# Performance work log

Measured on AMD Instinct MI355X. Metric: run time of the kernel, lower is better.

Reference implementation:

```python
import jax, jax.numpy as jnp
import numpy as np

N = 50000
E = 800000
NFEAT, NHID, NCLASS = 256, 128, 32


def setup_inputs() -> dict:
    key = jax.random.key(0)
    ks = jax.random.split(key, 8)
    x = jax.random.normal(ks[0], (N, NFEAT), dtype=jnp.float32)
    edge_src = jax.random.randint(ks[1], (E,), 0, N, dtype=jnp.int32)
    edge_dst = jax.random.randint(ks[2], (E,), 0, N, dtype=jnp.int32)
    edge_weight = jax.random.uniform(ks[3], (E,), dtype=jnp.float32)
    # Linear layer params (torch Linear: y = x @ W.T + b); store as [in, out]
    s1 = 1.0 / np.sqrt(NFEAT)
    s2 = 1.0 / np.sqrt(NHID)
    W1 = jax.random.uniform(ks[4], (NFEAT, NHID), jnp.float32, -s1, s1)
    b1 = jax.random.uniform(ks[5], (NHID,), jnp.float32, -s1, s1)
    W2 = jax.random.uniform(ks[6], (NHID, NCLASS), jnp.float32, -s2, s2)
    b2 = jax.random.uniform(ks[7], (NCLASS,), jnp.float32, -s2, s2)
    return {"x": x, "edge_src": edge_src, "edge_dst": edge_dst,
            "edge_weight": edge_weight, "W1": W1, "b1": b1, "W2": W2, "b2": b2}


def spmm(edge_src, edge_dst, edge_weight, h):
    # out[dst] += w * h[src]  -- sparse adjacency @ dense features
    msgs = edge_weight[:, None] * h[edge_src]          # [E, F]
    return jax.ops.segment_sum(msgs, edge_dst, num_segments=N)


def reference(x, edge_src, edge_dst, edge_weight, W1, b1, W2, b2):
    # GCN layer 1: Linear -> SpMM -> ReLU (dropout inactive in eval mode)
    h = x @ W1 + b1                                    # [N, NHID]
    h = spmm(edge_src, edge_dst, edge_weight, h)
    h = jax.nn.relu(h)
    # GCN layer 2: Linear -> SpMM
    h = h @ W2 + b2                                    # [N, NCLASS]
    out = spmm(edge_src, edge_dst, edge_weight, h)
    return out
```

## Files before the change

kernel.cpp:

```cpp
#include <hip/hip_runtime.h>

#define NFEAT 256
#define NHID 128
#define NCLASS 32

typedef __attribute__((ext_vector_type(8))) short short8;
typedef __attribute__((ext_vector_type(4))) float f32x4;
typedef __attribute__((ext_vector_type(4))) int int4v;

static __device__ __forceinline__ unsigned short f2bf(float f) {
    unsigned u = __float_as_uint(f);
    unsigned r = (u + 0x7fffu + ((u >> 16) & 1u)) >> 16;
    return (unsigned short)r;
}
static __device__ __forceinline__ float bf_lo(unsigned d) {
    return __uint_as_float(d << 16);
}
static __device__ __forceinline__ float bf_hi(unsigned d) {
    return __uint_as_float(d & 0xffff0000u);
}

__global__ __launch_bounds__(256) void prep_kernel(
    const float* __restrict__ W1, unsigned short* __restrict__ W1t,
    const int* __restrict__ dst, int* __restrict__ bkt_partial, int E, int shift)
{
    const int tid = threadIdx.x;
    if (blockIdx.x < 128) {
        int o = blockIdx.x * 256 + tid;
        int c = o >> 8, k = o & 255;
        W1t[o] = f2bf(W1[(size_t)k * NHID + c]);
    } else {
        __shared__ int h[256];
        const int kb = blockIdx.x - 128;
        h[tid] = 0;
        __syncthreads();
        for (int e = kb * 256 + tid; e < E; e += 256 * 256)
            atomicAdd(&h[dst[e] >> shift], 1);
        __syncthreads();
        bkt_partial[kb * 256 + tid] = h[tid];
    }
}

__global__ __launch_bounds__(256) void gemm1_mfma_kernel(
    const float* __restrict__ x, const unsigned short* __restrict__ W1t,
    const float* __restrict__ b1, unsigned short* __restrict__ h1b, int N)
{
    __shared__ unsigned short wt[128 * 256];
    __shared__ unsigned short xs[64 * 64];

    const int tid = threadIdx.x;
    const int lane = tid & 63;
    const int wv = tid >> 6;
    const int row0 = blockIdx.x * 64;
    const int l15 = lane & 15;
    const int l47 = lane >> 4;
    const int r7 = lane & 7;

    {
        const int4v* src = (const int4v*)W1t;
#pragma unroll
        for (int j = 0; j < 16; ++j) {
            int si = tid + j * 256;
            int c = si >> 5, s = si & 31;
            int sp = (s & 24) | ((s & 7) ^ (c & 7));
            int4v v = src[si];
            *(int4v*)&wt[c * 256 + sp * 8] = v;
        }
    }

    auto stage_x = [&](int t) {
#pragma unroll
        for (int j = 0; j < 2; ++j) {
            int si = tid + j * 256;
            int r = si >> 3, s = si & 7;
            int row = row0 + r;
            float4 v0 = make_float4(0.f, 0.f, 0.f, 0.f), v1 = v0;
            if (row < N) {
                const float4* xp = (const float4*)&x[(size_t)row * NFEAT + t * 64 + s * 8];
                v0 = xp[0]; v1 = xp[1];
            }
            int w0 = f2bf(v0.x) | ((unsigned)f2bf(v0.y) << 16);
            int w1 = f2bf(v0.z) | ((unsigned)f2bf(v0.w) << 16);
            int w2 = f2bf(v1.x) | ((unsigned)f2bf(v1.y) << 16);
            int w3 = f2bf(v1.z) | ((unsigned)f2bf(v1.w) << 16);
            int sp = s ^ (r & 7);
            int4v pv; pv[0] = w0; pv[1] = w1; pv[2] = w2; pv[3] = w3;
            *(int4v*)&xs[r * 64 + sp * 8] = pv;
        }
    };

    f32x4 acc[8];
#pragma unroll
    for (int cf = 0; cf < 8; ++cf)
#pragma unroll
        for (int r = 0; r < 4; ++r) acc[cf][r] = 0.f;

    stage_x(0);
    __syncthreads();

    const int arow = wv * 16 + l15;
#pragma unroll
    for (int t = 0; t < 4; ++t) {
        short8 af[2];
#pragma unroll
        for (int kf = 0; kf < 2; ++kf) {
            int slot = (kf * 4 + l47) ^ r7;
            af[kf] = *(const short8*)&xs[arow * 64 + slot * 8];
        }
#pragma unroll
        for (int cf = 0; cf < 8; ++cf) {
            const int brow = cf * 16 + l15;
#pragma unroll
            for (int kf = 0; kf < 2; ++kf) {
                int slot = t * 8 + ((kf * 4 + l47) ^ r7);
                short8 bfr = *(const short8*)&wt[brow * 256 + slot * 8];
                acc[cf] = __builtin_amdgcn_mfma_f32_16x16x32_bf16(af[kf], bfr, acc[cf], 0, 0, 0);
            }
        }
        __syncthreads();
        if (t < 3) {
            stage_x(t + 1);
            __syncthreads();
        }
    }

#pragma unroll
    for (int cf = 0; cf < 8; ++cf) {
        float bias = b1[cf * 16 + l15];
#pragma unroll
        for (int r = 0; r < 4; ++r) {
            int row = row0 + wv * 16 + l47 * 4 + r;
            if (row < N)
                h1b[(size_t)row * NHID + cf * 16 + l15] = f2bf(acc[cf][r] + bias);
        }
    }
}

__global__ __launch_bounds__(256) void bucket_scan_kernel(
    const int* __restrict__ bkt_partial, int* __restrict__ bkt_base,
    int* __restrict__ bkt_cursor)
{
    __shared__ int s[256];
    const int t = threadIdx.x;
    int v = 0;
    for (int k = 0; k < 256; ++k) v += bkt_partial[k * 256 + t];
    s[t] = v;
    __syncthreads();
    for (int off = 1; off < 256; off <<= 1) {
        int tv = (t >= off) ? s[t - off] : 0;
        __syncthreads();
        s[t] += tv;
        __syncthreads();
    }
    int excl = s[t] - v;
    bkt_base[t] = excl;
    bkt_cursor[t] = excl;
    if (t == 255) bkt_base[256] = s[255];
}

#define SC_EPT 16
__global__ __launch_bounds__(256) void bucket_scatter_kernel(
    const int* __restrict__ src, const int* __restrict__ dst,
    const float* __restrict__ w, int* __restrict__ bkt_cursor,
    uint2* __restrict__ bkt_edges, int E, int shift)
{
    __shared__ int h[256];
    __shared__ int base[256];
    const int tid = threadIdx.x;
    const int e0 = blockIdx.x * (256 * SC_EPT);
    h[tid] = 0;
    __syncthreads();
#pragma unroll
    for (int j = 0; j < SC_EPT; ++j) {
        int e = e0 + tid + j * 256;
        if (e < E) atomicAdd(&h[dst[e] >> shift], 1);
    }
    __syncthreads();
    int c = h[tid];
    base[tid] = c ? atomicAdd(&bkt_cursor[tid], c) : 0;
    __syncthreads();
    h[tid] = 0;
    __syncthreads();
#pragma unroll
    for (int j = 0; j < SC_EPT; ++j) {
        int e = e0 + tid + j * 256;
        if (e < E) {
            int d = dst[e];
            int b = d >> shift;
            int lp = atomicAdd(&h[b], 1);
            uint2 rec;
            rec.x = (unsigned)src[e] | ((unsigned)(d & ((1 << shift) - 1)) << 24);
            rec.y = __float_as_uint(w[e]);
            bkt_edges[base[b] + lp] = rec;
        }
    }
}

__global__ __launch_bounds__(256) void fine_scatter_kernel(
    const int* __restrict__ bkt_base, const uint2* __restrict__ bkt_edges,
    int* __restrict__ row_ptr, uint2* __restrict__ csr_e,
    int shift, int N, int E)
{
    __shared__ int h[256];
    __shared__ int cur[256];
    const int b = blockIdx.x;
    const int t = threadIdx.x;
    const int lo = bkt_base[b], hi = bkt_base[b + 1];
    const int dbase = b << shift;

    h[t] = 0;
    __syncthreads();
    for (int i = lo + t; i < hi; i += 256)
        atomicAdd(&h[bkt_edges[i].x >> 24], 1);
    __syncthreads();
    int v = h[t];
    __syncthreads();
    h[t] = v;
    __syncthreads();
    for (int off = 1; off < 256; off <<= 1) {
        int tv = (t >= off) ? h[t - off] : 0;
        __syncthreads();
        h[t] += tv;
        __syncthreads();
    }
    int excl = h[t] - v;
    {
        int r = dbase + t;
        if (r < N) row_ptr[r] = lo + excl;
    }
    if (b == 0 && t == 0) row_ptr[N] = E;
    cur[t] = lo + excl;
    __syncthreads();
    for (int i = lo + t; i < hi; i += 256) {
        uint2 rec = bkt_edges[i];
        int dl = rec.x >> 24;
        int pos = atomicAdd(&cur[dl], 1);
        uint2 o;
        o.x = rec.x & 0xFFFFFFu;
        o.y = rec.y;
        csr_e[pos] = o;
    }
}

__global__ __launch_bounds__(512) void spmm1_gemm2_kernel(
    const int* __restrict__ row_ptr, const uint2* __restrict__ csr_e,
    const unsigned short* __restrict__ h1b, const float* __restrict__ W2,
    const float* __restrict__ b2, unsigned* __restrict__ h2b, int N)
{
    __shared__ float w2s[NHID * NCLASS];
    __shared__ float hrow[8][NHID];
    const int tid = threadIdx.x;
#pragma unroll
    for (int j = 0; j < 8; ++j) {
        int idx = tid + j * 512;
        w2s[idx] = W2[idx];
    }
    __syncthreads();

    const int lane = tid & 63;
    const int wv = tid >> 6;
    const int row = __builtin_amdgcn_readfirstlane(blockIdx.x * 8 + wv);
    if (row >= N) return;

    const int e0 = row_ptr[row], e1 = row_ptr[row + 1];
    const size_t loff = (size_t)(lane * 2);
    float a0 = 0.f, a1 = 0.f;
    int e = e0;
    for (; e + 8 <= e1; e += 8) {
        uint2 r[8];
#pragma unroll
        for (int j = 0; j < 8; ++j) r[j] = csr_e[e + j];
        unsigned d[8];
#pragma unroll
        for (int j = 0; j < 8; ++j)
            d[j] = *(const unsigned*)(h1b + (size_t)r[j].x * NHID + loff);
#pragma unroll
        for (int j = 0; j < 8; ++j) {
            float w = __uint_as_float(r[j].y);
            a0 += w * bf_lo(d[j]); a1 += w * bf_hi(d[j]);
        }
    }
    for (; e + 2 <= e1; e += 2) {
        uint2 r0 = csr_e[e], r1 = csr_e[e + 1];
        unsigned d0 = *(const unsigned*)(h1b + (size_t)r0.x * NHID + loff);
        unsigned d1 = *(const unsigned*)(h1b + (size_t)r1.x * NHID + loff);
        float w0 = __uint_as_float(r0.y), w1 = __uint_as_float(r1.y);
        a0 += w0 * bf_lo(d0); a1 += w0 * bf_hi(d0);
        a0 += w1 * bf_lo(d1); a1 += w1 * bf_hi(d1);
    }
    if (e < e1) {
        uint2 r = csr_e[e];
        float w = __uint_as_float(r.y);
        unsigned d = *(const unsigned*)(h1b + (size_t)r.x * NHID + loff);
        a0 += w * bf_lo(d); a1 += w * bf_hi(d);
    }
    *(float2*)&hrow[wv][lane * 2] = make_float2(fmaxf(a0, 0.f), fmaxf(a1, 0.f));

    const int c = lane & 31;
    const int half = lane >> 5;
    const float* hw = &hrow[wv][half * 64];
    const float* wp = &w2s[(size_t)half * 64 * NCLASS + c];
    float acc = 0.f;
#pragma unroll
    for (int k = 0; k < 64; ++k)
        acc += hw[k] * wp[k * NCLASS];
    acc += __shfl(acc, lane ^ 32);
    float accb = acc + b2[c];
    float nb = __shfl(accb, lane ^ 1);
    if (half == 0 && (lane & 1) == 0) {
        unsigned u = (unsigned)f2bf(accb) | ((unsigned)f2bf(nb) << 16);
        h2b[(size_t)row * 16 + (lane >> 1)] = u;
    }
}

__global__ __launch_bounds__(256) void spmm2_kernel(
    const int* __restrict__ row_ptr, const uint2* __restrict__ csr_e,
    const unsigned* __restrict__ h2b, float* __restrict__ out, int N)
{
    const int li = threadIdx.x & 15;
    const int g = threadIdx.x >> 4;
    const int row = blockIdx.x * 16 + g;
    if (row >= N) return;
    const int e0 = row_ptr[row], e1 = row_ptr[row + 1];
    float a0 = 0.f, a1 = 0.f;
    int e = e0;
    for (; e + 8 <= e1; e += 8) {
        uint2 r[8];
#pragma unroll
        for (int j = 0; j < 8; ++j) r[j] = csr_e[e + j];
        unsigned d[8];
#pragma unroll
        for (int j = 0; j < 8; ++j) d[j] = h2b[(size_t)r[j].x * 16 + li];
#pragma unroll
        for (int j = 0; j < 8; ++j) {
            float w = __uint_as_float(r[j].y);
            a0 += w * bf_lo(d[j]); a1 += w * bf_hi(d[j]);
        }
    }
    for (; e + 2 <= e1; e += 2) {
        uint2 r0 = csr_e[e], r1 = csr_e[e + 1];
        unsigned d0 = h2b[(size_t)r0.x * 16 + li];
        unsigned d1 = h2b[(size_t)r1.x * 16 + li];
        float w0 = __uint_as_float(r0.y), w1 = __uint_as_float(r1.y);
        a0 += w0 * bf_lo(d0); a1 += w0 * bf_hi(d0);
        a0 += w1 * bf_lo(d1); a1 += w1 * bf_hi(d1);
    }
    if (e < e1) {
        uint2 r = csr_e[e];
        float w = __uint_as_float(r.y);
        unsigned d = h2b[(size_t)r.x * 16 + li];
        a0 += w * bf_lo(d); a1 += w * bf_hi(d);
    }
    *(float2*)&out[(size_t)row * NCLASS + li * 2] = make_float2(a0, a1);
}


extern "C" void kernel_launch(void* const* d_in, const int* in_sizes, int n_in,
                              void* d_out, int out_size, void* d_ws, size_t ws_size,
                              hipStream_t stream) {
    const float* x    = (const float*)d_in[0];
    const int*   esrc = (const int*)d_in[1];
    const int*   edst = (const int*)d_in[2];
    const float* ew   = (const float*)d_in[3];
    const float* W1   = (const float*)d_in[4];
    const float* b1   = (const float*)d_in[5];
    const float* W2   = (const float*)d_in[6];
    const float* b2   = (const float*)d_in[7];
    float* out = (float*)d_out;

    const int N = in_sizes[0] / NFEAT;
    const int E = in_sizes[1];

    int shift = 0;
    while (((N - 1) >> shift) >= 256) ++shift;
    const int NBKT = ((N - 1) >> shift) + 1;

    char* base = (char*)d_ws;
    size_t off = 0;
    auto take = [&](size_t bytes) -> void* {
        void* p = base + off;
        off += (bytes + 255) & ~(size_t)255;
        return p;
    };
    unsigned short* h1b = (unsigned short*)take((size_t)N * NHID * sizeof(unsigned short));
    unsigned* h2b  = (unsigned*)take((size_t)N * 16 * sizeof(unsigned));
    int*   row_ptr = (int*)take((size_t)(N + 1) * sizeof(int));
    int*   bkt_partial = (int*)take(256 * 256 * sizeof(int));
    int*   bkt_base    = (int*)take(257 * sizeof(int));
    int*   bkt_cursor  = (int*)take(256 * sizeof(int));
    uint2* bkt_edges   = (uint2*)take((size_t)E * sizeof(uint2));
    uint2* csr_e       = (uint2*)take((size_t)E * sizeof(uint2));
    unsigned short* W1t = (unsigned short*)take((size_t)NFEAT * NHID * sizeof(unsigned short));
    (void)ws_size; (void)n_in; (void)out_size;

    prep_kernel<<<384, 256, 0, stream>>>(W1, W1t, edst, bkt_partial, E, shift);
    gemm1_mfma_kernel<<<(N + 63) / 64, 256, 0, stream>>>(x, W1t, b1, h1b, N);
    bucket_scan_kernel<<<1, 256, 0, stream>>>(bkt_partial, bkt_base, bkt_cursor);
    bucket_scatter_kernel<<<(E + 256 * SC_EPT - 1) / (256 * SC_EPT), 256, 0, stream>>>(
        esrc, edst, ew, bkt_cursor, bkt_edges, E, shift);
    fine_scatter_kernel<<<NBKT, 256, 0, stream>>>(bkt_base, bkt_edges, row_ptr, csr_e,
                                                  shift, N, E);
    spmm1_gemm2_kernel<<<(N + 7) / 8, 512, 0, stream>>>(row_ptr, csr_e, h1b, W2, b2, h2b, N);
    spmm2_kernel<<<(N + 15) / 16, 256, 0, stream>>>(row_ptr, csr_e, h2b, out, N);
}
```

Measured before the change: 125.8 us.

## Vectorize SpMM gathers with edge-parallel lane groups and simplify bucket counting

Both SpMM kernels now split a wavefront into lane groups that each take a different edge and load 16-byte feature chunks, then reduce across groups with shuffles. This gives fewer, wider gathers and more edges in flight per row. Bucket counts are accumulated with global atomics into a 256-entry array, which removes the 256x256 partial-sum reduction in the scan kernel but adds a memset. The fine scatter runs 1024 threads per bucket block and the coarse scatter uses fewer edges per thread. The risks are shuffle-reduction overhead and idle lanes on low-degree rows, where average degree is about 16.

```diff
diff --git a/kernel.cpp b/kernel.cpp
--- a/kernel.cpp
+++ b/kernel.cpp
@@ -22,7 +22,7 @@
 
 __global__ __launch_bounds__(256) void prep_kernel(
     const float* __restrict__ W1, unsigned short* __restrict__ W1t,
-    const int* __restrict__ dst, int* __restrict__ bkt_partial, int E, int shift)
+    const int* __restrict__ dst, int* __restrict__ bkt_counts, int E, int shift)
 {
     const int tid = threadIdx.x;
     if (blockIdx.x < 128) {
@@ -37,7 +37,8 @@
         for (int e = kb * 256 + tid; e < E; e += 256 * 256)
             atomicAdd(&h[dst[e] >> shift], 1);
         __syncthreads();
-        bkt_partial[kb * 256 + tid] = h[tid];
+        int v = h[tid];
+        if (v) atomicAdd(&bkt_counts[tid], v);
     }
 }
 
@@ -137,13 +138,12 @@
 }
 
 __global__ __launch_bounds__(256) void bucket_scan_kernel(
-    const int* __restrict__ bkt_partial, int* __restrict__ bkt_base,
+    const int* __restrict__ bkt_counts, int* __restrict__ bkt_base,
     int* __restrict__ bkt_cursor)
 {
     __shared__ int s[256];
     const int t = threadIdx.x;
-    int v = 0;
-    for (int k = 0; k < 256; ++k) v += bkt_partial[k * 256 + t];
+    int v = bkt_counts[t];
     s[t] = v;
     __syncthreads();
     for (int off = 1; off < 256; off <<= 1) {
@@ -158,7 +158,7 @@
     if (t == 255) bkt_base[256] = s[255];
 }
 
-#define SC_EPT 16
+#define SC_EPT 8
 __global__ __launch_bounds__(256) void bucket_scatter_kernel(
     const int* __restrict__ src, const int* __restrict__ dst,
     const float* __restrict__ w, int* __restrict__ bkt_cursor,
@@ -196,7 +196,7 @@
     }
 }
 
-__global__ __launch_bounds__(256) void fine_scatter_kernel(
+__global__ __launch_bounds__(1024) void fine_scatter_kernel(
     const int* __restrict__ bkt_base, const uint2* __restrict__ bkt_edges,
     int* __restrict__ row_ptr, uint2* __restrict__ csr_e,
     int shift, int N, int E)
@@ -208,30 +208,27 @@
     const int lo = bkt_base[b], hi = bkt_base[b + 1];
     const int dbase = b << shift;
 
-    h[t] = 0;
-    __syncthreads();
-    for (int i = lo + t; i < hi; i += 256)
+    if (t < 256) h[t] = 0;
+    __syncthreads();
+    for (int i = lo + t; i < hi; i += 1024)
         atomicAdd(&h[bkt_edges[i].x >> 24], 1);
     __syncthreads();
-    int v = h[t];
-    __syncthreads();
-    h[t] = v;
-    __syncthreads();
+    int v = (t < 256) ? h[t] : 0;
     for (int off = 1; off < 256; off <<= 1) {
-        int tv = (t >= off) ? h[t - off] : 0;
-        __syncthreads();
-        h[t] += tv;
-        __syncthreads();
-    }
-    int excl = h[t] - v;
-    {
+        int tv = (t >= off && t < 256) ? h[t - off] : 0;
+        __syncthreads();
+        if (t < 256) h[t] += tv;
+        __syncthreads();
+    }
+    if (t < 256) {
+        int excl = h[t] - v;
         int r = dbase + t;
         if (r < N) row_ptr[r] = lo + excl;
+        cur[t] = lo + excl;
     }
     if (b == 0 && t == 0) row_ptr[N] = E;
-    cur[t] = lo + excl;
-    __syncthreads();
-    for (int i = lo + t; i < hi; i += 256) {
+    __syncthreads();
+    for (int i = lo + t; i < hi; i += 1024) {
         uint2 rec = bkt_edges[i];
         int dl = rec.x >> 24;
         int pos = atomicAdd(&cur[dl], 1);
@@ -262,39 +259,51 @@
     const int row = __builtin_amdgcn_readfirstlane(blockIdx.x * 8 + wv);
     if (row >= N) return;
 
+    const int grp = lane >> 4;
+    const int fl = lane & 15;
+
     const int e0 = row_ptr[row], e1 = row_ptr[row + 1];
-    const size_t loff = (size_t)(lane * 2);
-    float a0 = 0.f, a1 = 0.f;
+    float a[8];
+#pragma unroll
+    for (int i = 0; i < 8; ++i) a[i] = 0.f;
+
     int e = e0;
     for (; e + 8 <= e1; e += 8) {
-        uint2 r[8];
-#pragma unroll
-        for (int j = 0; j < 8; ++j) r[j] = csr_e[e + j];
-        unsigned d[8];
-#pragma unroll
-        for (int j = 0; j < 8; ++j)
-            d[j] = *(const unsigned*)(h1b + (size_t)r[j].x * NHID + loff);
-#pragma unroll
-        for (int j = 0; j < 8; ++j) {
-            float w = __uint_as_float(r[j].y);
-            a0 += w * bf_lo(d[j]); a1 += w * bf_hi(d[j]);
-        }
-    }
-    for (; e + 2 <= e1; e += 2) {
-        uint2 r0 = csr_e[e], r1 = csr_e[e + 1];
-        unsigned d0 = *(const unsigned*)(h1b + (size_t)r0.x * NHID + loff);
-        unsigned d1 = *(const unsigned*)(h1b + (size_t)r1.x * NHID + loff);
+        uint2 r0 = csr_e[e + grp];
+        uint2 r1 = csr_e[e + 4 + grp];
+        uint4 d0 = *(const uint4*)(h1b + (size_t)r0.x * NHID + fl * 8);
+        uint4 d1 = *(const uint4*)(h1b + (size_t)r1.x * NHID + fl * 8);
         float w0 = __uint_as_float(r0.y), w1 = __uint_as_float(r1.y);
-        a0 += w0 * bf_lo(d0); a1 += w0 * bf_hi(d0);
-        a0 += w1 * bf_lo(d1); a1 += w1 * bf_hi(d1);
-    }
-    if (e < e1) {
-        uint2 r = csr_e[e];
-        float w = __uint_as_float(r.y);
-        unsigned d = *(const unsigned*)(h1b + (size_t)r.x * NHID + loff);
-        a0 += w * bf_lo(d); a1 += w * bf_hi(d);
-    }
-    *(float2*)&hrow[wv][lane * 2] = make_float2(fmaxf(a0, 0.f), fmaxf(a1, 0.f));
+        a[0] += w0 * bf_lo(d0.x); a[1] += w0 * bf_hi(d0.x);
+        a[2] += w0 * bf_lo(d0.y); a[3] += w0 * bf_hi(d0.y);
+        a[4] += w0 * bf_lo(d0.z); a[5] += w0 * bf_hi(d0.z);
+        a[6] += w0 * bf_lo(d0.w); a[7] += w0 * bf_hi(d0.w);
+        a[0] += w1 * bf_lo(d1.x); a[1] += w1 * bf_hi(d1.x);
+        a[2] += w1 * bf_lo(d1.y); a[3] += w1 * bf_hi(d1.y);
+        a[4] += w1 * bf_lo(d1.z); a[5] += w1 * bf_hi(d1.z);
+        a[6] += w1 * bf_lo(d1.w); a[7] += w1 * bf_hi(d1.w);
+    }
+    for (; e < e1; e += 4) {
+        int idx = e + grp;
+        bool ok = idx < e1;
+        uint2 r = csr_e[ok ? idx : e1 - 1];
+        uint4 d = *(const uint4*)(h1b + (size_t)r.x * NHID + fl * 8);
+        float w = ok ? __uint_as_float(r.y) : 0.f;
+        a[0] += w * bf_lo(d.x); a[1] += w * bf_hi(d.x);
+        a[2] += w * bf_lo(d.y); a[3] += w * bf_hi(d.y);
+        a[4] += w * bf_lo(d.z); a[5] += w * bf_hi(d.z);
+        a[6] += w * bf_lo(d.w); a[7] += w * bf_hi(d.w);
+    }
+#pragma unroll
+    for (int i = 0; i < 8; ++i) {
+        a[i] += __shfl(a[i], lane ^ 16);
+        a[i] += __shfl(a[i], lane ^ 32);
+        a[i] = fmaxf(a[i], 0.f);
+    }
+    if (grp == 0) {
+        *(float4*)&hrow[wv][fl * 8]     = make_float4(a[0], a[1], a[2], a[3]);
+        *(float4*)&hrow[wv][fl * 8 + 4] = make_float4(a[4], a[5], a[6], a[7]);
+    }
 
     const int c = lane & 31;
     const int half = lane >> 5;
@@ -317,41 +326,51 @@
     const int* __restrict__ row_ptr, const uint2* __restrict__ csr_e,
     const unsigned* __restrict__ h2b, float* __restrict__ out, int N)
 {
-    const int li = threadIdx.x & 15;
-    const int g = threadIdx.x >> 4;
-    const int row = blockIdx.x * 16 + g;
+    const int lane = threadIdx.x & 63;
+    const int wv = threadIdx.x >> 6;
+    const int row = __builtin_amdgcn_readfirstlane(blockIdx.x * 4 + wv);
     if (row >= N) return;
+
+    const int grp = lane >> 2;
+    const int fl = lane & 3;
+
     const int e0 = row_ptr[row], e1 = row_ptr[row + 1];
-    float a0 = 0.f, a1 = 0.f;
+    float a[8];
+#pragma unroll
+    for (int i = 0; i < 8; ++i) a[i] = 0.f;
+
     int e = e0;
-    for (; e + 8 <= e1; e += 8) {
-        uint2 r[8];
-#pragma unroll
-        for (int j = 0; j < 8; ++j) r[j] = csr_e[e + j];
-        unsigned d[8];
-#pragma unroll
-        for (int j = 0; j < 8; ++j) d[j] = h2b[(size_t)r[j].x * 16 + li];
-#pragma unroll
-        for (int j = 0; j < 8; ++j) {
-            float w = __uint_as_float(r[j].y);
-            a0 += w * bf_lo(d[j]); a1 += w * bf_hi(d[j]);
-        }
-    }
-    for (; e + 2 <= e1; e += 2) {
-        uint2 r0 = csr_e[e], r1 = csr_e[e + 1];
-        unsigned d0 = h2b[(size_t)r0.x * 16 + li];
-        unsigned d1 = h2b[(size_t)r1.x * 16 + li];
-        float w0 = __uint_as_float(r0.y), w1 = __uint_as_float(r1.y);
-        a0 += w0 * bf_lo(d0); a1 += w0 * bf_hi(d0);
-        a0 += w1 * bf_lo(d1); a1 += w1 * bf_hi(d1);
+    for (; e + 16 <= e1; e += 16) {
+        uint2 r = csr_e[e + grp];
+        uint4 d = *(const uint4*)(h2b + (size_t)r.x * 16 + fl * 4);
+        float w = __uint_as_float(r.y);
+        a[0] += w * bf_lo(d.x); a[1] += w * bf_hi(d.x);
+        a[2] += w * bf_lo(d.y); a[3] += w * bf_hi(d.y);
+        a[4] += w * bf_lo(d.z); a[5] += w * bf_hi(d.z);
+        a[6] += w * bf_lo(d.w); a[7] += w * bf_hi(d.w);
     }
     if (e < e1) {
-        uint2 r = csr_e[e];
-        float w = __uint_as_float(r.y);
-        unsigned d = h2b[(size_t)r.x * 16 + li];
-        a0 += w * bf_lo(d); a1 += w * bf_hi(d);
-    }
-    *(float2*)&out[(size_t)row * NCLASS + li * 2] = make_float2(a0, a1);
+        int idx = e + grp;
+        bool ok = idx < e1;
+        uint2 r = csr_e[ok ? idx : e1 - 1];
+        uint4 d = *(const uint4*)(h2b + (size_t)r.x * 16 + fl * 4);
+        float w = ok ? __uint_as_float(r.y) : 0.f;
+        a[0] += w * bf_lo(d.x); a[1] += w * bf_hi(d.x);
+        a[2] += w * bf_lo(d.y); a[3] += w * bf_hi(d.y);
+        a[4] += w * bf_lo(d.z); a[5] += w * bf_hi(d.z);
+        a[6] += w * bf_lo(d.w); a[7] += w * bf_hi(d.w);
+    }
+#pragma unroll
+    for (int i = 0; i < 8; ++i) {
+        a[i] += __shfl(a[i], lane ^ 4);
+        a[i] += __shfl(a[i], lane ^ 8);
+        a[i] += __shfl(a[i], lane ^ 16);
+        a[i] += __shfl(a[i], lane ^ 32);
+    }
+    if (grp == 0) {
+        *(float4*)&out[(size_t)row * NCLASS + fl * 8]     = make_float4(a[0], a[1], a[2], a[3]);
+        *(float4*)&out[(size_t)row * NCLASS + fl * 8 + 4] = make_float4(a[4], a[5], a[6], a[7]);
+    }
 }
 
 
@@ -385,7 +404,7 @@
     unsigned short* h1b = (unsigned short*)take((size_t)N * NHID * sizeof(unsigned short));
     unsigned* h2b  = (unsigned*)take((size_t)N * 16 * sizeof(unsigned));
     int*   row_ptr = (int*)take((size_t)(N + 1) * sizeof(int));
-    int*   bkt_partial = (int*)take(256 * 256 * sizeof(int));
+    int*   bkt_counts  = (int*)take(256 * sizeof(int));
     int*   bkt_base    = (int*)take(257 * sizeof(int));
     int*   bkt_cursor  = (int*)take(256 * sizeof(int));
     uint2* bkt_edges   = (uint2*)take((size_t)E * sizeof(uint2));
@@ -393,13 +412,14 @@
     unsigned short* W1t = (unsigned short*)take((size_t)NFEAT * NHID * sizeof(unsigned short));
     (void)ws_size; (void)n_in; (void)out_size;
 
-    prep_kernel<<<384, 256, 0, stream>>>(W1, W1t, edst, bkt_partial, E, shift);
+    hipMemsetAsync(bkt_counts, 0, 256 * sizeof(int), stream);
+    prep_kernel<<<384, 256, 0, stream>>>(W1, W1t, edst, bkt_counts, E, shift);
     gemm1_mfma_kernel<<<(N + 63) / 64, 256, 0, stream>>>(x, W1t, b1, h1b, N);
-    bucket_scan_kernel<<<1, 256, 0, stream>>>(bkt_partial, bkt_base, bkt_cursor);
+    bucket_scan_kernel<<<1, 256, 0, stream>>>(bkt_counts, bkt_base, bkt_cursor);
     bucket_scatter_kernel<<<(E + 256 * SC_EPT - 1) / (256 * SC_EPT), 256, 0, stream>>>(
         esrc, edst, ew, bkt_cursor, bkt_edges, E, shift);
-    fine_scatter_kernel<<<NBKT, 256, 0, stream>>>(bkt_base, bkt_edges, row_ptr, csr_e,
-                                                  shift, N, E);
+    fine_scatter_kernel<<<NBKT, 1024, 0, stream>>>(bkt_base, bkt_edges, row_ptr, csr_e,
+                                                   shift, N, E);
     spmm1_gemm2_kernel<<<(N + 7) / 8, 512, 0, stream>>>(row_ptr, csr_e, h1b, W2, b2, h2b, N);
-    spmm2_kernel<<<(N + 15) / 16, 256, 0, stream>>>(row_ptr, csr_e, h2b, out, N);
-}
+    spmm2_kernel<<<(N + 3) / 4, 256, 0, stream>>>(row_ptr, csr_e, h2b, out, N);
+}
```

After: 137.0 us. 1.09x slower.

## Atomic bucket counts, wider fine scatter, swizzled float4 W2 for fused gemm2

Applied to the files above, without the earlier changes.

Bucket histogram partials are now reduced with global atomics into 256 counters, so the scan kernel no longer sums a 256x256 partial table. The fine scatter kernel runs 1024 threads per bucket to cover more edges per block. W2 is pre-transposed into an XOR-swizzled float4 layout so the fused spmm1/gemm2 kernel reads it with vector LDS loads and fewer bank conflicts. The coarse scatter also processes fewer edges per block. The cost is an extra memset launch and contended global atomics.

```diff
diff --git a/kernel.cpp b/kernel.cpp
--- a/kernel.cpp
+++ b/kernel.cpp
@@ -22,22 +22,37 @@
 
 __global__ __launch_bounds__(256) void prep_kernel(
     const float* __restrict__ W1, unsigned short* __restrict__ W1t,
-    const int* __restrict__ dst, int* __restrict__ bkt_partial, int E, int shift)
+    const float* __restrict__ W2, float4* __restrict__ w2t4,
+    const int* __restrict__ dst, int* __restrict__ bkt_counts, int E, int shift)
 {
     const int tid = threadIdx.x;
     if (blockIdx.x < 128) {
         int o = blockIdx.x * 256 + tid;
         int c = o >> 8, k = o & 255;
         W1t[o] = f2bf(W1[(size_t)k * NHID + c]);
+    } else if (blockIdx.x == 128) {
+#pragma unroll
+        for (int j = 0; j < 4; ++j) {
+            int o = tid + j * 256;
+            int c = o >> 5, sp = o & 31;
+            int s = sp ^ (c & 7);
+            float4 v;
+            v.x = W2[(size_t)(s * 4 + 0) * NCLASS + c];
+            v.y = W2[(size_t)(s * 4 + 1) * NCLASS + c];
+            v.z = W2[(size_t)(s * 4 + 2) * NCLASS + c];
+            v.w = W2[(size_t)(s * 4 + 3) * NCLASS + c];
+            w2t4[o] = v;
+        }
     } else {
         __shared__ int h[256];
-        const int kb = blockIdx.x - 128;
+        const int kb = blockIdx.x - 129;
         h[tid] = 0;
         __syncthreads();
         for (int e = kb * 256 + tid; e < E; e += 256 * 256)
             atomicAdd(&h[dst[e] >> shift], 1);
         __syncthreads();
-        bkt_partial[kb * 256 + tid] = h[tid];
+        int v = h[tid];
+        if (v) atomicAdd(&bkt_counts[tid], v);
     }
 }
 
@@ -137,13 +152,12 @@
 }
 
 __global__ __launch_bounds__(256) void bucket_scan_kernel(
-    const int* __restrict__ bkt_partial, int* __restrict__ bkt_base,
+    const int* __restrict__ bkt_counts, int* __restrict__ bkt_base,
     int* __restrict__ bkt_cursor)
 {
     __shared__ int s[256];
     const int t = threadIdx.x;
-    int v = 0;
-    for (int k = 0; k < 256; ++k) v += bkt_partial[k * 256 + t];
+    int v = bkt_counts[t];
     s[t] = v;
     __syncthreads();
     for (int off = 1; off < 256; off <<= 1) {
@@ -158,7 +172,7 @@
     if (t == 255) bkt_base[256] = s[255];
 }
 
-#define SC_EPT 16
+#define SC_EPT 8
 __global__ __launch_bounds__(256) void bucket_scatter_kernel(
     const int* __restrict__ src, const int* __restrict__ dst,
     const float* __restrict__ w, int* __restrict__ bkt_cursor,
@@ -196,7 +210,7 @@
     }
 }
 
-__global__ __launch_bounds__(256) void fine_scatter_kernel(
+__global__ __launch_bounds__(1024) void fine_scatter_kernel(
     const int* __restrict__ bkt_base, const uint2* __restrict__ bkt_edges,
     int* __restrict__ row_ptr, uint2* __restrict__ csr_e,
     int shift, int N, int E)
@@ -208,30 +222,27 @@
     const int lo = bkt_base[b], hi = bkt_base[b + 1];
     const int dbase = b << shift;
 
-    h[t] = 0;
-    __syncthreads();
-    for (int i = lo + t; i < hi; i += 256)
+    if (t < 256) h[t] = 0;
+    __syncthreads();
+    for (int i = lo + t; i < hi; i += 1024)
         atomicAdd(&h[bkt_edges[i].x >> 24], 1);
     __syncthreads();
-    int v = h[t];
-    __syncthreads();
-    h[t] = v;
-    __syncthreads();
+    int v = (t < 256) ? h[t] : 0;
     for (int off = 1; off < 256; off <<= 1) {
-        int tv = (t >= off) ? h[t - off] : 0;
-        __syncthreads();
-        h[t] += tv;
-        __syncthreads();
-    }
-    int excl = h[t] - v;
-    {
+        int tv = (t >= off && t < 256) ? h[t - off] : 0;
+        __syncthreads();
+        if (t < 256) h[t] += tv;
+        __syncthreads();
+    }
+    if (t < 256) {
+        int excl = h[t] - v;
         int r = dbase + t;
         if (r < N) row_ptr[r] = lo + excl;
+        cur[t] = lo + excl;
     }
     if (b == 0 && t == 0) row_ptr[N] = E;
-    cur[t] = lo + excl;
-    __syncthreads();
-    for (int i = lo + t; i < hi; i += 256) {
+    __syncthreads();
+    for (int i = lo + t; i < hi; i += 1024) {
         uint2 rec = bkt_edges[i];
         int dl = rec.x >> 24;
         int pos = atomicAdd(&cur[dl], 1);
@@ -244,16 +255,16 @@
 
 __global__ __launch_bounds__(512) void spmm1_gemm2_kernel(
     const int* __restrict__ row_ptr, const uint2* __restrict__ csr_e,
-    const unsigned short* __restrict__ h1b, const float* __restrict__ W2,
+    const unsigned short* __restrict__ h1b, const float4* __restrict__ w2t4,
     const float* __restrict__ b2, unsigned* __restrict__ h2b, int N)
 {
-    __shared__ float w2s[NHID * NCLASS];
+    __shared__ float4 w2s4[32 * 32];
     __shared__ float hrow[8][NHID];
     const int tid = threadIdx.x;
 #pragma unroll
-    for (int j = 0; j < 8; ++j) {
+    for (int j = 0; j < 2; ++j) {
         int idx = tid + j * 512;
-        w2s[idx] = W2[idx];
+        w2s4[idx] = w2t4[idx];
     }
     __syncthreads();
 
@@ -298,12 +309,16 @@
 
     const int c = lane & 31;
     const int half = lane >> 5;
-    const float* hw = &hrow[wv][half * 64];
-    const float* wp = &w2s[(size_t)half * 64 * NCLASS + c];
+    const float4* hb = (const float4*)&hrow[wv][half * 64];
+    const int cs7 = c & 7;
     float acc = 0.f;
 #pragma unroll
-    for (int k = 0; k < 64; ++k)
-        acc += hw[k] * wp[k * NCLASS];
+    for (int k4 = 0; k4 < 16; ++k4) {
+        int s = half * 16 + k4;
+        float4 w4 = w2s4[c * 32 + (s ^ cs7)];
+        float4 h4 = hb[k4];
+        acc += h4.x * w4.x + h4.y * w4.y + h4.z * w4.z + h4.w * w4.w;
+    }
     acc += __shfl(acc, lane ^ 32);
     float accb = acc + b2[c];
     float nb = __shfl(accb, lane ^ 1);
@@ -385,21 +400,23 @@
     unsigned short* h1b = (unsigned short*)take((size_t)N * NHID * sizeof(unsigned short));
     unsigned* h2b  = (unsigned*)take((size_t)N * 16 * sizeof(unsigned));
     int*   row_ptr = (int*)take((size_t)(N + 1) * sizeof(int));
-    int*   bkt_partial = (int*)take(256 * 256 * sizeof(int));
+    int*   bkt_counts  = (int*)take(256 * sizeof(int));
     int*   bkt_base    = (int*)take(257 * sizeof(int));
     int*   bkt_cursor  = (int*)take(256 * sizeof(int));
     uint2* bkt_edges   = (uint2*)take((size_t)E * sizeof(uint2));
     uint2* csr_e       = (uint2*)take((size_t)E * sizeof(uint2));
     unsigned short* W1t = (unsigned short*)take((size_t)NFEAT * NHID * sizeof(unsigned short));
+    float4* w2t4       = (float4*)take(1024 * sizeof(float4));
     (void)ws_size; (void)n_in; (void)out_size;
 
-    prep_kernel<<<384, 256, 0, stream>>>(W1, W1t, edst, bkt_partial, E, shift);
+    hipMemsetAsync(bkt_counts, 0, 256 * sizeof(int), stream);
+    prep_kernel<<<385, 256, 0, stream>>>(W1, W1t, W2, w2t4, edst, bkt_counts, E, shift);
     gemm1_mfma_kernel<<<(N + 63) / 64, 256, 0, stream>>>(x, W1t, b1, h1b, N);
-    bucket_scan_kernel<<<1, 256, 0, stream>>>(bkt_partial, bkt_base, bkt_cursor);
+    bucket_scan_kernel<<<1, 256, 0, stream>>>(bkt_counts, bkt_base, bkt_cursor);
     bucket_scatter_kernel<<<(E + 256 * SC_EPT - 1) / (256 * SC_EPT), 256, 0, stream>>>(
         esrc, edst, ew, bkt_cursor, bkt_edges, E, shift);
-    fine_scatter_kernel<<<NBKT, 256, 0, stream>>>(bkt_base, bkt_edges, row_ptr, csr_e,
-                                                  shift, N, E);
-    spmm1_gemm2_kernel<<<(N + 7) / 8, 512, 0, stream>>>(row_ptr, csr_e, h1b, W2, b2, h2b, N);
+    fine_scatter_kernel<<<NBKT, 1024, 0, stream>>>(bkt_base, bkt_edges, row_ptr, csr_e,
+                                                   shift, N, E);
+    spmm1_gemm2_kernel<<<(N + 7) / 8, 512, 0, stream>>>(row_ptr, csr_e, h1b, w2t4, b2, h2b, N);
     spmm2_kernel<<<(N + 15) / 16, 256, 0, stream>>>(row_ptr, csr_e, h2b, out, N);
 }
```

Result: faster. 119.8 us (-4.7%).

## Restructure CSR build with per-chunk prefix offsets, persistent GEMM1, wider fine scatter

Applied to the files above, without the earlier changes.

The bucket histogram now works on contiguous per-block edge chunks. A single scan produces per-chunk prefix offsets, so the bucket scatter no longer needs a second histogram pass or global atomics on bucket cursors. The fine scatter runs with 1024 threads per block, GEMM1 becomes a persistent 256-block loop that loads W1 into LDS once per block, and GEMM1 is moved after the CSR build. The SpMM1 tail gains a 4-edge unrolled step. The trade-off is serial per-thread loops in the scan kernel, less parallelism in bucket_scatter, and a different kernel launch order.

```diff
diff --git a/kernel.cpp b/kernel.cpp
--- a/kernel.cpp
+++ b/kernel.cpp
@@ -22,7 +22,8 @@
 
 __global__ __launch_bounds__(256) void prep_kernel(
     const float* __restrict__ W1, unsigned short* __restrict__ W1t,
-    const int* __restrict__ dst, int* __restrict__ bkt_partial, int E, int shift)
+    const int* __restrict__ dst, int* __restrict__ bkt_partial,
+    int E, int CE, int shift)
 {
     const int tid = threadIdx.x;
     if (blockIdx.x < 128) {
@@ -32,119 +33,29 @@
     } else {
         __shared__ int h[256];
         const int kb = blockIdx.x - 128;
+        const int start = kb * CE;
+        const int end = min(start + CE, E);
         h[tid] = 0;
         __syncthreads();
-        for (int e = kb * 256 + tid; e < E; e += 256 * 256)
+        for (int e = start + tid; e < end; e += 256)
             atomicAdd(&h[dst[e] >> shift], 1);
         __syncthreads();
         bkt_partial[kb * 256 + tid] = h[tid];
     }
 }
 
-__global__ __launch_bounds__(256) void gemm1_mfma_kernel(
-    const float* __restrict__ x, const unsigned short* __restrict__ W1t,
-    const float* __restrict__ b1, unsigned short* __restrict__ h1b, int N)
-{
-    __shared__ unsigned short wt[128 * 256];
-    __shared__ unsigned short xs[64 * 64];
-
-    const int tid = threadIdx.x;
-    const int lane = tid & 63;
-    const int wv = tid >> 6;
-    const int row0 = blockIdx.x * 64;
-    const int l15 = lane & 15;
-    const int l47 = lane >> 4;
-    const int r7 = lane & 7;
-
-    {
-        const int4v* src = (const int4v*)W1t;
-#pragma unroll
-        for (int j = 0; j < 16; ++j) {
-            int si = tid + j * 256;
-            int c = si >> 5, s = si & 31;
-            int sp = (s & 24) | ((s & 7) ^ (c & 7));
-            int4v v = src[si];
-            *(int4v*)&wt[c * 256 + sp * 8] = v;
-        }
-    }
-
-    auto stage_x = [&](int t) {
-#pragma unroll
-        for (int j = 0; j < 2; ++j) {
-            int si = tid + j * 256;
-            int r = si >> 3, s = si & 7;
-            int row = row0 + r;
-            float4 v0 = make_float4(0.f, 0.f, 0.f, 0.f), v1 = v0;
-            if (row < N) {
-                const float4* xp = (const float4*)&x[(size_t)row * NFEAT + t * 64 + s * 8];
-                v0 = xp[0]; v1 = xp[1];
-            }
-            int w0 = f2bf(v0.x) | ((unsigned)f2bf(v0.y) << 16);
-            int w1 = f2bf(v0.z) | ((unsigned)f2bf(v0.w) << 16);
-            int w2 = f2bf(v1.x) | ((unsigned)f2bf(v1.y) << 16);
-            int w3 = f2bf(v1.z) | ((unsigned)f2bf(v1.w) << 16);
-            int sp = s ^ (r & 7);
-            int4v pv; pv[0] = w0; pv[1] = w1; pv[2] = w2; pv[3] = w3;
-            *(int4v*)&xs[r * 64 + sp * 8] = pv;
-        }
-    };
-
-    f32x4 acc[8];
-#pragma unroll
-    for (int cf = 0; cf < 8; ++cf)
-#pragma unroll
-        for (int r = 0; r < 4; ++r) acc[cf][r] = 0.f;
-
-    stage_x(0);
-    __syncthreads();
-
-    const int arow = wv * 16 + l15;
-#pragma unroll
-    for (int t = 0; t < 4; ++t) {
-        short8 af[2];
-#pragma unroll
-        for (int kf = 0; kf < 2; ++kf) {
-            int slot = (kf * 4 + l47) ^ r7;
-            af[kf] = *(const short8*)&xs[arow * 64 + slot * 8];
-        }
-#pragma unroll
-        for (int cf = 0; cf < 8; ++cf) {
-            const int brow = cf * 16 + l15;
-#pragma unroll
-            for (int kf = 0; kf < 2; ++kf) {
-                int slot = t * 8 + ((kf * 4 + l47) ^ r7);
-                short8 bfr = *(const short8*)&wt[brow * 256 + slot * 8];
-                acc[cf] = __builtin_amdgcn_mfma_f32_16x16x32_bf16(af[kf], bfr, acc[cf], 0, 0, 0);
-            }
-        }
-        __syncthreads();
-        if (t < 3) {
-            stage_x(t + 1);
-            __syncthreads();
-        }
-    }
-
-#pragma unroll
-    for (int cf = 0; cf < 8; ++cf) {
-        float bias = b1[cf * 16 + l15];
-#pragma unroll
-        for (int r = 0; r < 4; ++r) {
-            int row = row0 + wv * 16 + l47 * 4 + r;
-            if (row < N)
-                h1b[(size_t)row * NHID + cf * 16 + l15] = f2bf(acc[cf][r] + bias);
-        }
-    }
-}
-
-__global__ __launch_bounds__(256) void bucket_scan_kernel(
-    const int* __restrict__ bkt_partial, int* __restrict__ bkt_base,
-    int* __restrict__ bkt_cursor)
+__global__ __launch_bounds__(256) void scan_kernel(
+    const int* __restrict__ bkt_partial, int* __restrict__ chunk_pre,
+    int* __restrict__ bkt_base, int E)
 {
     __shared__ int s[256];
     const int t = threadIdx.x;
-    int v = 0;
-    for (int k = 0; k < 256; ++k) v += bkt_partial[k * 256 + t];
-    s[t] = v;
+    int run = 0;
+    for (int kb = 0; kb < 256; ++kb) {
+        chunk_pre[kb * 256 + t] = run;
+        run += bkt_partial[kb * 256 + t];
+    }
+    s[t] = run;
     __syncthreads();
     for (int off = 1; off < 256; off <<= 1) {
         int tv = (t >= off) ? s[t - off] : 0;
@@ -152,51 +63,36 @@
         s[t] += tv;
         __syncthreads();
     }
-    int excl = s[t] - v;
-    bkt_base[t] = excl;
-    bkt_cursor[t] = excl;
+    bkt_base[t] = s[t] - run;
     if (t == 255) bkt_base[256] = s[255];
 }
 
-#define SC_EPT 16
 __global__ __launch_bounds__(256) void bucket_scatter_kernel(
     const int* __restrict__ src, const int* __restrict__ dst,
-    const float* __restrict__ w, int* __restrict__ bkt_cursor,
-    uint2* __restrict__ bkt_edges, int E, int shift)
-{
-    __shared__ int h[256];
-    __shared__ int base[256];
+    const float* __restrict__ w, const int* __restrict__ bkt_base,
+    const int* __restrict__ chunk_pre, uint2* __restrict__ bkt_edges,
+    int E, int CE, int shift)
+{
+    __shared__ int cur[256];
     const int tid = threadIdx.x;
-    const int e0 = blockIdx.x * (256 * SC_EPT);
-    h[tid] = 0;
-    __syncthreads();
-#pragma unroll
-    for (int j = 0; j < SC_EPT; ++j) {
-        int e = e0 + tid + j * 256;
-        if (e < E) atomicAdd(&h[dst[e] >> shift], 1);
-    }
-    __syncthreads();
-    int c = h[tid];
-    base[tid] = c ? atomicAdd(&bkt_cursor[tid], c) : 0;
-    __syncthreads();
-    h[tid] = 0;
-    __syncthreads();
-#pragma unroll
-    for (int j = 0; j < SC_EPT; ++j) {
-        int e = e0 + tid + j * 256;
-        if (e < E) {
-            int d = dst[e];
-            int b = d >> shift;
-            int lp = atomicAdd(&h[b], 1);
-            uint2 rec;
-            rec.x = (unsigned)src[e] | ((unsigned)(d & ((1 << shift) - 1)) << 24);
-            rec.y = __float_as_uint(w[e]);
-            bkt_edges[base[b] + lp] = rec;
-        }
-    }
-}
-
-__global__ __launch_bounds__(256) void fine_scatter_kernel(
+    const int kb = blockIdx.x;
+    cur[tid] = bkt_base[tid] + chunk_pre[kb * 256 + tid];
+    __syncthreads();
+    const int start = kb * CE;
+    const int end = min(start + CE, E);
+    const unsigned lmask = (1u << shift) - 1u;
+    for (int e = start + tid; e < end; e += 256) {
+        int d = dst[e];
+        int b = d >> shift;
+        int pos = atomicAdd(&cur[b], 1);
+        uint2 rec;
+        rec.x = (unsigned)src[e] | (((unsigned)d & lmask) << 24);
+        rec.y = __float_as_uint(w[e]);
+        bkt_edges[pos] = rec;
+    }
+}
+
+__global__ __launch_bounds__(1024) void fine_scatter_kernel(
     const int* __restrict__ bkt_base, const uint2* __restrict__ bkt_edges,
     int* __restrict__ row_ptr, uint2* __restrict__ csr_e,
     int shift, int N, int E)
@@ -208,30 +104,27 @@
     const int lo = bkt_base[b], hi = bkt_base[b + 1];
     const int dbase = b << shift;
 
-    h[t] = 0;
-    __syncthreads();
-    for (int i = lo + t; i < hi; i += 256)
+    if (t < 256) h[t] = 0;
+    __syncthreads();
+    for (int i = lo + t; i < hi; i += 1024)
         atomicAdd(&h[bkt_edges[i].x >> 24], 1);
     __syncthreads();
-    int v = h[t];
-    __syncthreads();
-    h[t] = v;
-    __syncthreads();
+    int v = (t < 256) ? h[t] : 0;
     for (int off = 1; off < 256; off <<= 1) {
-        int tv = (t >= off) ? h[t - off] : 0;
-        __syncthreads();
-        h[t] += tv;
-        __syncthreads();
-    }
-    int excl = h[t] - v;
-    {
+        int tv = (t >= off && t < 256) ? h[t - off] : 0;
+        __syncthreads();
+        if (t < 256) h[t] += tv;
+        __syncthreads();
+    }
+    if (t < 256) {
+        int excl = h[t] - v;
         int r = dbase + t;
         if (r < N) row_ptr[r] = lo + excl;
+        cur[t] = lo + excl;
     }
     if (b == 0 && t == 0) row_ptr[N] = E;
-    cur[t] = lo + excl;
-    __syncthreads();
-    for (int i = lo + t; i < hi; i += 256) {
+    __syncthreads();
+    for (int i = lo + t; i < hi; i += 1024) {
         uint2 rec = bkt_edges[i];
         int dl = rec.x >> 24;
         int pos = atomicAdd(&cur[dl], 1);
@@ -242,6 +135,106 @@
     }
 }
 
+__global__ __launch_bounds__(256) void gemm1_mfma_kernel(
+    const float* __restrict__ x, const unsigned short* __restrict__ W1t,
+    const float* __restrict__ b1, unsigned short* __restrict__ h1b, int N)
+{
+    __shared__ unsigned short wt[128 * 256];
+    __shared__ unsigned short xs[64 * 64];
+
+    const int tid = threadIdx.x;
+    const int lane = tid & 63;
+    const int wv = tid >> 6;
+    const int l15 = lane & 15;
+    const int l47 = lane >> 4;
+    const int r7 = lane & 7;
+
+    {
+        const int4v* src = (const int4v*)W1t;
+#pragma unroll
+        for (int j = 0; j < 16; ++j) {
+            int si = tid + j * 256;
+            int c = si >> 5, s = si & 31;
+            int sp = (s & 24) | ((s & 7) ^ (c & 7));
+            int4v v = src[si];
+            *(int4v*)&wt[c * 256 + sp * 8] = v;
+        }
+    }
+
+    const int ntiles = (N + 63) >> 6;
+    for (int tile = blockIdx.x; tile < ntiles; tile += gridDim.x) {
+        const int row0 = tile * 64;
+
+        auto stage_x = [&](int t) {
+#pragma unroll
+            for (int j = 0; j < 2; ++j) {
+                int si = tid + j * 256;
+                int r = si >> 3, s = si & 7;
+                int row = row0 + r;
+                float4 v0 = make_float4(0.f, 0.f, 0.f, 0.f), v1 = v0;
+                if (row < N) {
+                    const float4* xp = (const float4*)&x[(size_t)row * NFEAT + t * 64 + s * 8];
+                    v0 = xp[0]; v1 = xp[1];
+                }
+                int w0 = f2bf(v0.x) | ((unsigned)f2bf(v0.y) << 16);
+                int w1 = f2bf(v0.z) | ((unsigned)f2bf(v0.w) << 16);
+                int w2 = f2bf(v1.x) | ((unsigned)f2bf(v1.y) << 16);
+                int w3 = f2bf(v1.z) | ((unsigned)f2bf(v1.w) << 16);
+                int sp = s ^ (r & 7);
+                int4v pv; pv[0] = w0; pv[1] = w1; pv[2] = w2; pv[3] = w3;
+                *(int4v*)&xs[r * 64 + sp * 8] = pv;
+            }
+        };
+
+        f32x4 acc[8];
+#pragma unroll
+        for (int cf = 0; cf < 8; ++cf)
+#pragma unroll
+            for (int r = 0; r < 4; ++r) acc[cf][r] = 0.f;
+
+        stage_x(0);
+        __syncthreads();
+
+        const int arow = wv * 16 + l15;
+#pragma unroll
+        for (int t = 0; t < 4; ++t) {
+            short8 af[2];
+#pragma unroll
+            for (int kf = 0; kf < 2; ++kf) {
+                int slot = (kf * 4 + l47) ^ r7;
+                af[kf] = *(const short8*)&xs[arow * 64 + slot * 8];
+            }
+#pragma unroll
+            for (int cf = 0; cf < 8; ++cf) {
+                const int brow = cf * 16 + l15;
+#pragma unroll
+                for (int kf = 0; kf < 2; ++kf) {
+                    int slot = t * 8 + ((kf * 4 + l47) ^ r7);
+                    short8 bfr = *(const short8*)&wt[brow * 256 + slot * 8];
+                    acc[cf] = __builtin_amdgcn_mfma_f32_16x16x32_bf16(af[kf], bfr, acc[cf], 0, 0, 0);
+                }
+            }
+            __syncthreads();
+            if (t < 3) {
+                stage_x(t + 1);
+                __syncthreads();
+            }
+        }
+
+#pragma unroll
+        for (int cf = 0; cf < 8; ++cf) {
+            float bias = b1[cf * 16 + l15];
+#pragma unroll
+            for (int r = 0; r < 4; ++r) {
+                int row = row0 + wv * 16 + l47 * 4 + r;
+                if (row < N)
+                    h1b[(size_t)row * NHID + cf * 16 + l15] = f2bf(acc[cf][r] + bias);
+            }
+        }
+        __syncthreads();
+    }
+}
+
 __global__ __launch_bounds__(512) void spmm1_gemm2_kernel(
     const int* __restrict__ row_ptr, const uint2* __restrict__ csr_e,
     const unsigned short* __restrict__ h1b, const float* __restrict__ W2,
@@ -280,13 +273,29 @@
             a0 += w * bf_lo(d[j]); a1 += w * bf_hi(d[j]);
         }
     }
-    for (; e + 2 <= e1; e += 2) {
+    if (e + 4 <= e1) {
+        uint2 r[4];
+#pragma unroll
+        for (int j = 0; j < 4; ++j) r[j] = csr_e[e + j];
+        unsigned d[4];
+#pragma unroll
+        for (int j = 0; j < 4; ++j)
+            d[j] = *(const unsigned*)(h1b + (size_t)r[j].x * NHID + loff);
+#pragma unroll
+        for (int j = 0; j < 4; ++j) {
+            float w = __uint_as_float(r[j].y);
+            a0 += w * bf_lo(d[j]); a1 += w * bf_hi(d[j]);
+        }
+        e += 4;
+    }
+    if (e + 2 <= e1) {
         uint2 r0 = csr_e[e], r1 = csr_e[e + 1];
         unsigned d0 = *(const unsigned*)(h1b + (size_t)r0.x * NHID + loff);
         unsigned d1 = *(const unsigned*)(h1b + (size_t)r1.x * NHID + loff);
         float w0 = __uint_as_float(r0.y), w1 = __uint_as_float(r1.y);
         a0 += w0 * bf_lo(d0); a1 += w0 * bf_hi(d0);
         a0 += w1 * bf_lo(d1); a1 += w1 * bf_hi(d1);
+        e += 2;
     }
     if (e < e1) {
         uint2 r = csr_e[e];
@@ -297,9 +306,9 @@
     *(float2*)&hrow[wv][lane * 2] = make_float2(fmaxf(a0, 0.f), fmaxf(a1, 0.f));
 
     const int c = lane & 31;
-    const int half = lane >> 5;
-    const float* hw = &hrow[wv][half * 64];
-    const float* wp = &w2s[(size_t)half * 64 * NCLASS + c];
+    const int kh = lane >> 5;
+    const float* hw = &hrow[wv][kh * 64];
+    const float* wp = &w2s[(size_t)kh * 64 * NCLASS + c];
     float acc = 0.f;
 #pragma unroll
     for (int k = 0; k < 64; ++k)
@@ -307,7 +316,7 @@
     acc += __shfl(acc, lane ^ 32);
     float accb = acc + b2[c];
     float nb = __shfl(accb, lane ^ 1);
-    if (half == 0 && (lane & 1) == 0) {
+    if (kh == 0 && (lane & 1) == 0) {
         unsigned u = (unsigned)f2bf(accb) | ((unsigned)f2bf(nb) << 16);
         h2b[(size_t)row * 16 + (lane >> 1)] = u;
     }
@@ -374,6 +383,7 @@
     int shift = 0;
     while (((N - 1) >> shift) >= 256) ++shift;
     const int NBKT = ((N - 1) >> shift) + 1;
+    const int CE = (E + 255) / 256;
 
     char* base = (char*)d_ws;
     size_t off = 0;
@@ -386,20 +396,20 @@
     unsigned* h2b  = (unsigned*)take((size_t)N * 16 * sizeof(unsigned));
     int*   row_ptr = (int*)take((size_t)(N + 1) * sizeof(int));
     int*   bkt_partial = (int*)take(256 * 256 * sizeof(int));
+    int*   chunk_pre   = (int*)take(256 * 256 * sizeof(int));
     int*   bkt_base    = (int*)take(257 * sizeof(int));
-    int*   bkt_cursor  = (int*)take(256 * sizeof(int));
     uint2* bkt_edges   = (uint2*)take((size_t)E * sizeof(uint2));
     uint2* csr_e       = (uint2*)take((size_t)E * sizeof(uint2));
     unsigned short* W1t = (unsigned short*)take((size_t)NFEAT * NHID * sizeof(unsigned short));
     (void)ws_size; (void)n_in; (void)out_size;
 
-    prep_kernel<<<384, 256, 0, stream>>>(W1, W1t, edst, bkt_partial, E, shift);
-    gemm1_mfma_kernel<<<(N + 63) / 64, 256, 0, stream>>>(x, W1t, b1, h1b, N);
-    bucket_scan_kernel<<<1, 256, 0, stream>>>(bkt_partial, bkt_base, bkt_cursor);
-    bucket_scatter_kernel<<<(E + 256 * SC_EPT - 1) / (256 * SC_EPT), 256, 0, stream>>>(
-        esrc, edst, ew, bkt_cursor, bkt_edges, E, shift);
-    fine_scatter_kernel<<<NBKT, 256, 0, stream>>>(bkt_base, bkt_edges, row_ptr, csr_e,
-                                                  shift, N, E);
+    prep_kernel<<<384, 256, 0, stream>>>(W1, W1t, edst, bkt_partial, E, CE, shift);
+    scan_kernel<<<1, 256, 0, stream>>>(bkt_partial, chunk_pre, bkt_base, E);
+    bucket_scatter_kernel<<<256, 256, 0, stream>>>(esrc, edst, ew, bkt_base, chunk_pre,
+                                                   bkt_edges, E, CE, shift);
+    fine_scatter_kernel<<<NBKT, 1024, 0, stream>>>(bkt_base, bkt_edges, row_ptr, csr_e,
+                                                   shift, N, E);
+    gemm1_mfma_kernel<<<256, 256, 0, stream>>>(x, W1t, b1, h1b, N);
     spmm1_gemm2_kernel<<<(N + 7) / 8, 512, 0, stream>>>(row_ptr, csr_e, h1b, W2, b2, h2b, N);
     spmm2_kernel<<<(N + 15) / 16, 256, 0, stream>>>(row_ptr, csr_e, h2b, out, N);
 }
```

Measured after the change: 116.0 us. -7.8%, faster.
